# Optimization experiments

Hardware: AMD Instinct MI355X
Metric: run time of the kernel (lower is better)

## Reference

```python
import jax, jax.numpy as jnp
import numpy as np

D = 1024
H = 16
HD = D // H
FF = 4 * D

def layer_norm(x, g, b, eps=1e-5):
    mu = jnp.mean(x, axis=-1, keepdims=True)
    var = jnp.var(x, axis=-1, keepdims=True)
    return (x - mu) * jax.lax.rsqrt(var + eps) * g + b

def setup_inputs() -> dict:
    key = jax.random.key(0)
    ks = jax.random.split(key, 8)
    s = 0.02
    return {
        "x": jax.random.normal(ks[0], (2, 2048, D), jnp.float32),
        "ln1_g": jnp.ones((D,), jnp.float32),
        "ln1_b": jnp.zeros((D,), jnp.float32),
        "w_qkv": jax.random.normal(ks[1], (3 * D, D), jnp.float32) * s,
        "b_qkv": jnp.zeros((3 * D,), jnp.float32),
        "w_proj": jax.random.normal(ks[2], (D, D), jnp.float32) * s,
        "b_proj": jnp.zeros((D,), jnp.float32),
        "ln2_g": jnp.ones((D,), jnp.float32),
        "ln2_b": jnp.zeros((D,), jnp.float32),
        "w_fc1": jax.random.normal(ks[3], (FF, D), jnp.float32) * s,
        "b_fc1": jnp.zeros((FF,), jnp.float32),
        "w_fc2": jax.random.normal(ks[4], (D, FF), jnp.float32) * s,
        "b_fc2": jnp.zeros((D,), jnp.float32),
    }

def reference(x, ln1_g, ln1_b, w_qkv, b_qkv, w_proj, b_proj,
              ln2_g, ln2_b, w_fc1, b_fc1, w_fc2, b_fc2):
    B, N, C = x.shape
    scale = HD ** -0.5
    # --- attention branch (pre-norm) ---
    h = layer_norm(x, ln1_g, ln1_b)
    qkv = h @ w_qkv.T + b_qkv                      # [B,N,3D]
    qkv = qkv.reshape(B, N, 3, H, HD).transpose(2, 0, 3, 1, 4)
    q, k, v = qkv[0], qkv[1], qkv[2]               # [B,H,N,HD]
    attn = jnp.einsum('bhnd,bhmd->bhnm', q, k) * scale
    attn = jax.nn.softmax(attn, axis=-1)
    o = jnp.einsum('bhnm,bhmd->bhnd', attn, v)     # [B,H,N,HD]
    o = o.transpose(0, 2, 1, 3).reshape(B, N, C)
    x = x + (o @ w_proj.T + b_proj)
    # --- FFN branch (pre-norm) ---
    h = layer_norm(x, ln2_g, ln2_b)
    h = jax.nn.gelu(h @ w_fc1.T + b_fc1, approximate=False)
    x = x + (h @ w_fc2.T + b_fc2)
    return x
```

## Files before the change

kernel.cpp:

```cpp
#include <hip/hip_runtime.h>

typedef __attribute__((ext_vector_type(8))) short short8;
typedef __attribute__((ext_vector_type(4))) float f32x4;

static __device__ __forceinline__ unsigned short f2bf(float f){
  unsigned u = __float_as_uint(f);
  u += 0x7FFF + ((u >> 16) & 1);
  return (unsigned short)(u >> 16);
}

static __device__ __forceinline__ f32x4 MF(short8 a, short8 b, f32x4 c){
  return __builtin_amdgcn_mfma_f32_16x16x32_bf16(a, b, c, 0, 0, 0);
}

#define GL16(g, l) __builtin_amdgcn_global_load_lds( \
    (const __attribute__((address_space(1))) void*)(g), \
    (__attribute__((address_space(3))) void*)(l), 16, 0, 0)

#define SBAR { __builtin_amdgcn_sched_barrier(0); __builtin_amdgcn_s_barrier(); __builtin_amdgcn_sched_barrier(0); }

__global__ __launch_bounds__(256) void cvt_all(
    const float* __restrict__ a0, const float* __restrict__ a1,
    const float* __restrict__ a2, const float* __restrict__ a3,
    unsigned short* __restrict__ o0, unsigned short* __restrict__ o1,
    unsigned short* __restrict__ o2, unsigned short* __restrict__ o3){
  int i = blockIdx.x * 256 + threadIdx.x;
  const float* src; unsigned short* dst; int off;
  if (i < 786432)       { src = a0; dst = o0; off = i; }
  else if (i < 1048576) { src = a1; dst = o1; off = i - 786432; }
  else if (i < 2097152) { src = a2; dst = o2; off = i - 1048576; }
  else                  { src = a3; dst = o3; off = i - 2097152; }
  float4 v = reinterpret_cast<const float4*>(src)[off];
  ushort4 o;
  o.x = f2bf(v.x); o.y = f2bf(v.y); o.z = f2bf(v.z); o.w = f2bf(v.w);
  reinterpret_cast<ushort4*>(dst)[off] = o;
}

__global__ __launch_bounds__(256) void ln_bf16(const float* __restrict__ x,
    const float* __restrict__ g, const float* __restrict__ b,
    unsigned short* __restrict__ out){
  int row = blockIdx.x, t = threadIdx.x;
  const float* xr = x + (size_t)row * 1024;
  float4 xv = reinterpret_cast<const float4*>(xr)[t];
  float s  = xv.x + xv.y + xv.z + xv.w;
  float sq = xv.x*xv.x + xv.y*xv.y + xv.z*xv.z + xv.w*xv.w;
  #pragma unroll
  for (int m = 32; m >= 1; m >>= 1){ s += __shfl_xor(s, m); sq += __shfl_xor(sq, m); }
  __shared__ float ss[4], ssq[4];
  int w = t >> 6, lane = t & 63;
  if (lane == 0){ ss[w] = s; ssq[w] = sq; }
  __syncthreads();
  s  = ss[0] + ss[1] + ss[2] + ss[3];
  sq = ssq[0] + ssq[1] + ssq[2] + ssq[3];
  float mu = s * (1.f/1024.f);
  float rs = rsqrtf(sq * (1.f/1024.f) - mu*mu + 1e-5f);
  float4 gv = reinterpret_cast<const float4*>(g)[t];
  float4 bv = reinterpret_cast<const float4*>(b)[t];
  ushort4 o;
  o.x = f2bf((xv.x - mu) * rs * gv.x + bv.x);
  o.y = f2bf((xv.y - mu) * rs * gv.y + bv.y);
  o.z = f2bf((xv.z - mu) * rs * gv.z + bv.z);
  o.w = f2bf((xv.w - mu) * rs * gv.w + bv.w);
  reinterpret_cast<ushort4*>(out + (size_t)row * 1024)[t] = o;
}

template<int EPI>
__global__ __launch_bounds__(512, 2) void gemm8p(
    const unsigned short* __restrict__ A,
    const unsigned short* __restrict__ B,
    const float* __restrict__ bias,
    void* __restrict__ C,
    int M, int N, int K)
{
  __shared__ __attribute__((aligned(16))) short As[2 * 256 * 64];
  __shared__ __attribute__((aligned(16))) short Bs[2 * 256 * 64];
  const int NT = K >> 6;
  int tid = threadIdx.x, lane = tid & 63, wave = tid >> 6;
  int wm = wave >> 2, wn = wave & 3;
  int l15 = lane & 15, hi = lane >> 4;
  int hi2 = hi ^ (((l15 >> 2) & 1) << 1);
  int bm = blockIdx.y * 256, bn = blockIdx.x * 256;
  int lr = lane >> 3;
  int sg8 = ((lane & 7) ^ ((lane >> 5) << 1)) * 8;
  int rb0 = wave * 16;

  f32x4 acc[8][4] = {};
  short8 aR[4][2], bA[2][2], bB[2][2];

  auto stage = [&](int T, int h){
    if (T >= NT) return;
    const unsigned short* src = (h < 2) ? (A + (size_t)(bm + ((h & 1) << 7)) * K)
                                        : (B + (size_t)(bn + ((h & 1) << 7)) * K);
    short* dst = ((h < 2) ? As : Bs) + ((T & 1) << 14) + ((h & 1) << 13);
    const unsigned short* s = src + (size_t)(rb0 + lr) * K + (T << 6) + sg8;
    GL16(s, dst + rb0 * 64);
    GL16(s + (size_t)8 * K, dst + (rb0 + 8) * 64);
  };
  auto LDA = [&](const short* Ab, int m, int kk){
    int R = wm * 128 + m * 16 + l15;
    return *(const short8*)(Ab + R * 64 + kk * 32 + hi2 * 8);
  };
  auto LDB = [&](const short* Bb, int n, int kk){
    int R = wn * 64 + n * 16 + l15;
    return *(const short8*)(Bb + R * 64 + kk * 32 + hi2 * 8);
  };

  stage(0, 0); stage(0, 1); stage(0, 2); stage(0, 3);
  stage(1, 0); stage(1, 1);
  asm volatile("s_waitcnt vmcnt(4)" ::: "memory");
  SBAR;

  for (int i = 0; i < (NT >> 1); ++i){
    int t0 = 2 * i, t1 = t0 + 1;
    const short* A0 = As;            const short* B0 = Bs;
    const short* A1 = As + 16384;    const short* B1 = Bs + 16384;
    #pragma unroll
    for (int m = 0; m < 4; m++){ aR[m][0] = LDA(A0, m, 0); aR[m][1] = LDA(A0, m, 1); }
    #pragma unroll
    for (int n = 0; n < 2; n++){ bA[n][0] = LDB(B0, n, 0); bA[n][1] = LDB(B0, n, 1); }
    __builtin_amdgcn_sched_barrier(0);
    stage(t1, 2);
    SBAR;
    __builtin_amdgcn_s_setprio(1);
    #pragma unroll
    for (int m = 0; m < 4; m++)
      #pragma unroll
      for (int n = 0; n < 2; n++)
        #pragma unroll
        for (int kk = 0; kk < 2; kk++) acc[m][n] = MF(aR[m][kk], bA[n][kk], acc[m][n]);
    __builtin_amdgcn_s_setprio(0);
    SBAR;
    #pragma unroll
    for (int n = 0; n < 2; n++){ bB[n][0] = LDB(B0, n + 2, 0); bB[n][1] = LDB(B0, n + 2, 1); }
    __builtin_amdgcn_sched_barrier(0);
    stage(t1, 3);
    SBAR;
    __builtin_amdgcn_s_setprio(1);
    #pragma unroll
    for (int m = 0; m < 4; m++)
      #pragma unroll
      for (int n = 0; n < 2; n++)
        #pragma unroll
        for (int kk = 0; kk < 2; kk++) acc[m][n + 2] = MF(aR[m][kk], bB[n][kk], acc[m][n + 2]);
    __builtin_amdgcn_s_setprio(0);
    SBAR;
    #pragma unroll
    for (int m = 0; m < 4; m++){ aR[m][0] = LDA(A0, m + 4, 0); aR[m][1] = LDA(A0, m + 4, 1); }
    __builtin_amdgcn_sched_barrier(0);
    stage(t0 + 2, 0);
    SBAR;
    __builtin_amdgcn_s_setprio(1);
    #pragma unroll
    for (int m = 0; m < 4; m++)
      #pragma unroll
      for (int n = 0; n < 2; n++)
        #pragma unroll
        for (int kk = 0; kk < 2; kk++) acc[m + 4][n] = MF(aR[m][kk], bA[n][kk], acc[m + 4][n]);
    __builtin_amdgcn_s_setprio(0);
    SBAR;
    stage(t0 + 2, 1);
    SBAR;
    __builtin_amdgcn_s_setprio(1);
    #pragma unroll
    for (int m = 0; m < 4; m++)
      #pragma unroll
      for (int n = 0; n < 2; n++)
        #pragma unroll
        for (int kk = 0; kk < 2; kk++) acc[m + 4][n + 2] = MF(aR[m][kk], bB[n][kk], acc[m + 4][n + 2]);
    __builtin_amdgcn_s_setprio(0);
    asm volatile("s_waitcnt vmcnt(4)" ::: "memory");
    SBAR;
    #pragma unroll
    for (int m = 0; m < 4; m++){ aR[m][0] = LDA(A1, m, 0); aR[m][1] = LDA(A1, m, 1); }
    #pragma unroll
    for (int n = 0; n < 2; n++){ bA[n][0] = LDB(B1, n, 0); bA[n][1] = LDB(B1, n, 1); }
    __builtin_amdgcn_sched_barrier(0);
    stage(t0 + 2, 2);
    SBAR;
    __builtin_amdgcn_s_setprio(1);
    #pragma unroll
    for (int m = 0; m < 4; m++)
      #pragma unroll
      for (int n = 0; n < 2; n++)
        #pragma unroll
        for (int kk = 0; kk < 2; kk++) acc[m][n] = MF(aR[m][kk], bA[n][kk], acc[m][n]);
    __builtin_amdgcn_s_setprio(0);
    SBAR;
    #pragma unroll
    for (int n = 0; n < 2; n++){ bB[n][0] = LDB(B1, n + 2, 0); bB[n][1] = LDB(B1, n + 2, 1); }
    __builtin_amdgcn_sched_barrier(0);
    stage(t0 + 2, 3);
    SBAR;
    __builtin_amdgcn_s_setprio(1);
    #pragma unroll
    for (int m = 0; m < 4; m++)
      #pragma unroll
      for (int n = 0; n < 2; n++)
        #pragma unroll
        for (int kk = 0; kk < 2; kk++) acc[m][n + 2] = MF(aR[m][kk], bB[n][kk], acc[m][n + 2]);
    __builtin_amdgcn_s_setprio(0);
    SBAR;
    #pragma unroll
    for (int m = 0; m < 4; m++){ aR[m][0] = LDA(A1, m + 4, 0); aR[m][1] = LDA(A1, m + 4, 1); }
    __builtin_amdgcn_sched_barrier(0);
    stage(t0 + 3, 0);
    SBAR;
    __builtin_amdgcn_s_setprio(1);
    #pragma unroll
    for (int m = 0; m < 4; m++)
      #pragma unroll
      for (int n = 0; n < 2; n++)
        #pragma unroll
        for (int kk = 0; kk < 2; kk++) acc[m + 4][n] = MF(aR[m][kk], bA[n][kk], acc[m + 4][n]);
    __builtin_amdgcn_s_setprio(0);
    SBAR;
    stage(t0 + 3, 1);
    SBAR;
    __builtin_amdgcn_s_setprio(1);
    #pragma unroll
    for (int m = 0; m < 4; m++)
      #pragma unroll
      for (int n = 0; n < 2; n++)
        #pragma unroll
        for (int kk = 0; kk < 2; kk++) acc[m + 4][n + 2] = MF(aR[m][kk], bB[n][kk], acc[m + 4][n + 2]);
    __builtin_amdgcn_s_setprio(0);
    asm volatile("s_waitcnt vmcnt(4)" ::: "memory");
    SBAR;
  }

  #pragma unroll
  for (int m = 0; m < 8; m++){
    int row = bm + wm * 128 + m * 16 + hi * 4;
    #pragma unroll
    for (int n = 0; n < 4; n++){
      int col = bn + wn * 64 + n * 16 + l15;
      float bv = bias[col];
      #pragma unroll
      for (int j = 0; j < 4; j++){
        float v = acc[m][n][j] + bv;
        if (EPI == 1){
          float w2 = v * v;
          float t = exp2f(v * fmaf(w2, 0.10294322f, 2.3022078f));
          float r = __builtin_amdgcn_rcpf(1.f + t);
          v = v - v * r;
        }
        ((unsigned short*)C)[(size_t)(row + j) * N + col] = f2bf(v);
      }
    }
  }
}

template<int EPI>
__global__ __launch_bounds__(512) void gemm_ks(
    const unsigned short* __restrict__ A,
    const unsigned short* __restrict__ B,
    const float* __restrict__ bias,
    const float* __restrict__ resid,
    void* __restrict__ C,
    int M, int N, int K)
{
  __shared__ __attribute__((aligned(16))) short As[2][2][128 * 64];
  __shared__ __attribute__((aligned(16))) short Bs[2][2][128 * 64];
  const int NS = K >> 7;
  int tid = threadIdx.x, lane = tid & 63, wave = tid >> 6;
  int kg = wave >> 2;
  int ws = wave & 3;
  int wm = ws >> 1, wn = ws & 1;
  int l15 = lane & 15, hi = lane >> 4, l7 = l15 & 7;
  int lin = blockIdx.y * 8 + blockIdx.x;
  int xcd = lin & 7, idx = lin >> 3;
  int bm = (xcd * 4 + (idx >> 3)) * 128;
  int bn = (idx & 7) * 128;
  int lr = lane >> 3;
  int sega = ((lane & 7) ^ lr) * 8;
  f32x4 acc[4][4] = {};

  auto stage = [&](int buf, int k0){
    #pragma unroll
    for (int j = 0; j < 4; j++){
      int row = ws * 32 + j * 8;
      GL16(A + (size_t)(bm + row + lr) * K + k0 + sega, &As[kg][buf][row * 64]);
      GL16(B + (size_t)(bn + row + lr) * K + k0 + sega, &Bs[kg][buf][row * 64]);
    }
  };
  auto LDA = [&](int buf, int m, int kk){
    int R = wm * 64 + m * 16 + l15;
    return *(const short8*)(&As[kg][buf][R * 64 + (((kk << 2) | hi) ^ l7) * 8]);
  };
  auto LDB = [&](int buf, int n, int kk){
    int R = wn * 64 + n * 16 + l15;
    return *(const short8*)(&Bs[kg][buf][R * 64 + (((kk << 2) | hi) ^ l7) * 8]);
  };

  stage(0, kg * 64);
  for (int j = 0; j < NS; j++){
    int cur = j & 1;
    if (j + 1 < NS){
      stage(cur ^ 1, (j + 1) * 128 + kg * 64);
      asm volatile("s_waitcnt vmcnt(8)" ::: "memory");
    } else {
      asm volatile("s_waitcnt vmcnt(0)" ::: "memory");
    }
    SBAR;
    #pragma unroll
    for (int kk = 0; kk < 2; kk++){
      short8 af[4], bf[4];
      #pragma unroll
      for (int m = 0; m < 4; m++) af[m] = LDA(cur, m, kk);
      #pragma unroll
      for (int n = 0; n < 4; n++) bf[n] = LDB(cur, n, kk);
      __builtin_amdgcn_s_setprio(1);
      #pragma unroll
      for (int m = 0; m < 4; m++)
        #pragma unroll
        for (int n = 0; n < 4; n++)
          acc[m][n] = MF(af[m], bf[n], acc[m][n]);
      __builtin_amdgcn_s_setprio(0);
    }
    SBAR;
  }

  float* red = (float*)&As[0][0][0];
  if (kg == 1){
    #pragma unroll
    for (int m = 0; m < 4; m++)
      #pragma unroll
      for (int n = 0; n < 4; n++)
        #pragma unroll
        for (int j = 0; j < 4; j++)
          red[ws * 4096 + (m * 16 + hi * 4 + j) * 64 + n * 16 + l15] = acc[m][n][j];
  }
  __syncthreads();
  if (kg == 0){
    #pragma unroll
    for (int m = 0; m < 4; m++){
      int row = bm + wm * 64 + m * 16 + hi * 4;
      #pragma unroll
      for (int n = 0; n < 4; n++){
        int col = bn + wn * 64 + n * 16 + l15;
        float bv = bias[col];
        #pragma unroll
        for (int j = 0; j < 4; j++){
          float v = acc[m][n][j] + red[ws * 4096 + (m * 16 + hi * 4 + j) * 64 + n * 16 + l15] + bv;
          int r = row + j;
          if (EPI == 2){
            ((float*)C)[(size_t)r * N + col] = v + resid[(size_t)r * N + col];
          } else {
            ((unsigned short*)C)[(size_t)r * N + col] = f2bf(v);
          }
        }
      }
    }
  }
}

__global__ __launch_bounds__(512) void attn_fwd(const unsigned short* __restrict__ qkv,
                                                unsigned short* __restrict__ o){
  __shared__ __attribute__((aligned(16))) short K_lds[2][64*64];
  __shared__ __attribute__((aligned(16))) short V_lds[2][64*64];
  __shared__ __attribute__((aligned(16))) short P_lds[8][16*64];
  int tid = threadIdx.x, wave = tid >> 6, lane = tid & 63;
  int l15 = lane & 15, hi = lane >> 4, l7 = l15 & 7;
  int bid = blockIdx.x;
  int swz = (bid & 7) * 64 + (bid >> 3);
  int qt = swz & 15, bh = swz >> 4;
  int b = bh >> 4, h = bh & 15;
  const unsigned short* qbase = qkv + (size_t)b * 2048 * 3072 + h * 64;
  const unsigned short* kbase = qbase + 1024;
  const unsigned short* vbase = qbase + 2048;
  int qrow = qt * 128 + wave * 16 + l15;
  short8 qf0 = *(const short8*)(qbase + (size_t)qrow * 3072 + hi * 8);
  short8 qf1 = *(const short8*)(qbase + (size_t)qrow * 3072 + 32 + hi * 8);
  #pragma unroll
  for (int j = 0; j < 8; j++){
    float q0 = __uint_as_float((unsigned)(unsigned short)qf0[j] << 16) * 0.18033688f;
    float q1 = __uint_as_float((unsigned)(unsigned short)qf1[j] << 16) * 0.18033688f;
    qf0[j] = (short)f2bf(q0);
    qf1[j] = (short)f2bf(q1);
  }
  short8 ones8;
  #pragma unroll
  for (int j = 0; j < 8; j++) ones8[j] = (short)0x3F80;
  int vt = tid - 256;
  int ki0 = tid * 2, ki1 = ki0 + 1;
  int kr0 = ki0 >> 3, ks0 = ki0 & 7;
  int kr1 = ki1 >> 3, ks1 = ki1 & 7;
  int kp = vt & 31, ds8 = (vt >> 5) & 7;
  int vcg = kp >> 2, vwi = (2 * kp) & 7;
  f32x4 accO[4] = {};
  f32x4 lacc = {};
  short* Pw = &P_lds[wave][0];

  auto kv_load = [&](int kt, short8& s0, short8& s1){
    if (vt < 0){
      s0 = *(const short8*)(kbase + (size_t)(kt + kr0) * 3072 + ks0 * 8);
      s1 = *(const short8*)(kbase + (size_t)(kt + kr1) * 3072 + ks1 * 8);
    } else {
      const unsigned short* vr = vbase + (size_t)(kt + 2 * kp) * 3072 + ds8 * 8;
      s0 = *(const short8*)vr;
      s1 = *(const short8*)(vr + 3072);
    }
  };
  auto kv_store = [&](int buf, short8 s0, short8 s1){
    if (vt < 0){
      *(short8*)(&K_lds[buf][kr0 * 64 + ((ks0 ^ (kr0 & 7)) << 3)]) = s0;
      *(short8*)(&K_lds[buf][kr1 * 64 + ((ks1 ^ (kr1 & 7)) << 3)]) = s1;
    } else {
      unsigned* Vw = (unsigned*)&V_lds[buf][0];
      #pragma unroll
      for (int j = 0; j < 8; j++){
        int d = ds8 * 8 + j;
        int sa = d * 64 + ((vcg ^ (d & 7)) << 3) + vwi;
        Vw[sa >> 1] = (unsigned)(unsigned short)s0[j] | ((unsigned)(unsigned short)s1[j] << 16);
      }
    }
  };

  {
    short8 s0, s1;
    kv_load(0, s0, s1);
    kv_store(0, s0, s1);
    __syncthreads();
  }

  for (int t = 0; t < 32; t++){
    int cur = t & 1;
    const short* Kc = &K_lds[cur][0];
    const short* Vc = &V_lds[cur][0];
    short8 s0, s1;
    if (t < 31) kv_load((t + 1) * 64, s0, s1);
    f32x4 sacc[4];
    __builtin_amdgcn_s_setprio(1);
    #pragma unroll
    for (int kb = 0; kb < 4; kb++){
      f32x4 s = {};
      short8 ka = *(const short8*)(Kc + (kb * 16 + l15) * 64 + ((hi ^ l7) << 3));
      s = __builtin_amdgcn_mfma_f32_16x16x32_bf16(ka, qf0, s, 0, 0, 0);
      short8 kb_ = *(const short8*)(Kc + (kb * 16 + l15) * 64 + (((4 + hi) ^ l7) << 3));
      s = __builtin_amdgcn_mfma_f32_16x16x32_bf16(kb_, qf1, s, 0, 0, 0);
      sacc[kb] = s;
    }
    __builtin_amdgcn_s_setprio(0);
    unsigned pu[8];
    #pragma unroll
    for (int kb = 0; kb < 4; kb++){
      unsigned u0 = (unsigned)(int)fmaf(sacc[kb][0], 128.f, 16248.6f);
      unsigned u1 = (unsigned)(int)fmaf(sacc[kb][1], 128.f, 16248.6f);
      unsigned u2 = (unsigned)(int)fmaf(sacc[kb][2], 128.f, 16248.6f);
      unsigned u3 = (unsigned)(int)fmaf(sacc[kb][3], 128.f, 16248.6f);
      pu[kb * 2]     = u0 | (u1 << 16);
      pu[kb * 2 + 1] = u2 | (u3 << 16);
    }
    #pragma unroll
    for (int kb = 0; kb < 4; kb++){
      int sa = l15 * 64 + ((((kb << 1) | (hi >> 1)) ^ l7) << 3) + ((hi & 1) << 2);
      *(uint2*)(Pw + sa) = make_uint2(pu[kb * 2], pu[kb * 2 + 1]);
    }
    __builtin_amdgcn_s_setprio(1);
    #pragma unroll
    for (int kb2 = 0; kb2 < 2; kb2++){
      short8 pf = *(const short8*)(Pw + l15 * 64 + ((((kb2 << 2) | hi) ^ l7) << 3));
      #pragma unroll
      for (int db = 0; db < 4; db++){
        short8 vf = *(const short8*)(Vc + (db * 16 + l15) * 64 + ((((kb2 << 2) | hi) ^ l7) << 3));
        accO[db] = __builtin_amdgcn_mfma_f32_16x16x32_bf16(vf, pf, accO[db], 0, 0, 0);
      }
      lacc = __builtin_amdgcn_mfma_f32_16x16x32_bf16(ones8, pf, lacc, 0, 0, 0);
    }
    __builtin_amdgcn_s_setprio(0);
    if (t < 31){
      kv_store(cur ^ 1, s0, s1);
      __syncthreads();
    }
  }
  float inv = 1.f / lacc[0];
  unsigned short* ob = o + (size_t)(b * 2048 + qt * 128 + wave * 16 + l15) * 1024 + h * 64;
  #pragma unroll
  for (int db = 0; db < 4; db++){
    ushort4 w;
    w.x = f2bf(accO[db][0] * inv);
    w.y = f2bf(accO[db][1] * inv);
    w.z = f2bf(accO[db][2] * inv);
    w.w = f2bf(accO[db][3] * inv);
    *(ushort4*)(ob + db * 16 + hi * 4) = w;
  }
}

extern "C" void kernel_launch(void* const* d_in, const int* in_sizes, int n_in,
                              void* d_out, int out_size, void* d_ws, size_t ws_size,
                              hipStream_t stream){
  const float* x      = (const float*)d_in[0];
  const float* ln1_g  = (const float*)d_in[1];
  const float* ln1_b  = (const float*)d_in[2];
  const float* w_qkv  = (const float*)d_in[3];
  const float* b_qkv  = (const float*)d_in[4];
  const float* w_proj = (const float*)d_in[5];
  const float* b_proj = (const float*)d_in[6];
  const float* ln2_g  = (const float*)d_in[7];
  const float* ln2_b  = (const float*)d_in[8];
  const float* w_fc1  = (const float*)d_in[9];
  const float* b_fc1  = (const float*)d_in[10];
  const float* w_fc2  = (const float*)d_in[11];
  const float* b_fc2  = (const float*)d_in[12];
  float* out = (float*)d_out;
  char* ws = (char*)d_ws;
  const size_t MB = 1024 * 1024;
  unsigned short* h     = (unsigned short*)(ws);
  unsigned short* qkv   = (unsigned short*)(ws + 8*MB);
  unsigned short* ob    = (unsigned short*)(ws + 32*MB);
  float*          x1    = (float*)(ws + 40*MB);
  unsigned short* f     = (unsigned short*)(ws + 56*MB);
  unsigned short* wqkvb = (unsigned short*)(ws + 88*MB);
  unsigned short* wprojb= (unsigned short*)(ws + 94*MB);
  unsigned short* wfc1b = (unsigned short*)(ws + 96*MB);
  unsigned short* wfc2b = (unsigned short*)(ws + 104*MB);

  cvt_all<<<12288, 256, 0, stream>>>(w_qkv, w_proj, w_fc1, w_fc2,
                                     wqkvb, wprojb, wfc1b, wfc2b);

  ln_bf16<<<4096, 256, 0, stream>>>(x, ln1_g, ln1_b, h);
  gemm8p<0><<<dim3(12, 16), 512, 0, stream>>>(h, wqkvb, b_qkv, qkv, 4096, 3072, 1024);
  attn_fwd<<<512, 512, 0, stream>>>(qkv, ob);
  gemm_ks<2><<<dim3(8, 32), 512, 0, stream>>>(ob, wprojb, b_proj, x, x1, 4096, 1024, 1024);
  ln_bf16<<<4096, 256, 0, stream>>>(x1, ln2_g, ln2_b, h);
  gemm8p<1><<<dim3(16, 16), 512, 0, stream>>>(h, wfc1b, b_fc1, f, 4096, 4096, 1024);
  gemm_ks<2><<<dim3(8, 32), 512, 0, stream>>>(f, wfc2b, b_fc2, x1, out, 4096, 1024, 4096);
}
```

Measured before the change: 220.6 us.

## Run FC2 as split-K gemm8p with bf16 partials and separate reduce kernel

```diff
diff --git a/kernel.cpp b/kernel.cpp
--- a/kernel.cpp
+++ b/kernel.cpp
@@ -64,13 +64,32 @@
   reinterpret_cast<ushort4*>(out + (size_t)row * 1024)[t] = o;
 }
 
+__global__ __launch_bounds__(256) void reduce4(
+    const unsigned short* __restrict__ p, const float* __restrict__ bias,
+    const float* __restrict__ resid, float* __restrict__ out){
+  int i = blockIdx.x * 256 + threadIdx.x;
+  int e = i * 4, col = e & 1023;
+  float4 r = *reinterpret_cast<const float4*>(resid + e);
+  float4 bv = *reinterpret_cast<const float4*>(bias + col);
+  float s0 = r.x + bv.x, s1 = r.y + bv.y, s2 = r.z + bv.z, s3 = r.w + bv.w;
+  #pragma unroll
+  for (int sp = 0; sp < 4; sp++){
+    ushort4 u = *reinterpret_cast<const ushort4*>(p + (size_t)sp * 4194304 + e);
+    s0 += __uint_as_float((unsigned)u.x << 16);
+    s1 += __uint_as_float((unsigned)u.y << 16);
+    s2 += __uint_as_float((unsigned)u.z << 16);
+    s3 += __uint_as_float((unsigned)u.w << 16);
+  }
+  *reinterpret_cast<float4*>(out + e) = make_float4(s0, s1, s2, s3);
+}
+
 template<int EPI>
 __global__ __launch_bounds__(512, 2) void gemm8p(
     const unsigned short* __restrict__ A,
     const unsigned short* __restrict__ B,
     const float* __restrict__ bias,
     void* __restrict__ C,
-    int M, int N, int K)
+    int M, int N, int K, int LDK)
 {
   __shared__ __attribute__((aligned(16))) short As[2 * 256 * 64];
   __shared__ __attribute__((aligned(16))) short Bs[2 * 256 * 64];
@@ -80,6 +99,10 @@
   int l15 = lane & 15, hi = lane >> 4;
   int hi2 = hi ^ (((l15 >> 2) & 1) << 1);
   int bm = blockIdx.y * 256, bn = blockIdx.x * 256;
+  size_t koff = (size_t)blockIdx.z * K;
+  A += koff; B += koff;
+  unsigned short* Cp = (unsigned short*)C;
+  if (EPI == 3) Cp += (size_t)blockIdx.z * M * N;
   int lr = lane >> 3;
   int sg8 = ((lane & 7) ^ ((lane >> 5) << 1)) * 8;
   int rb0 = wave * 16;
@@ -89,12 +112,12 @@
 
   auto stage = [&](int T, int h){
     if (T >= NT) return;
-    const unsigned short* src = (h < 2) ? (A + (size_t)(bm + ((h & 1) << 7)) * K)
-                                        : (B + (size_t)(bn + ((h & 1) << 7)) * K);
+    const unsigned short* src = (h < 2) ? (A + (size_t)(bm + ((h & 1) << 7)) * LDK)
+                                        : (B + (size_t)(bn + ((h & 1) << 7)) * LDK);
     short* dst = ((h < 2) ? As : Bs) + ((T & 1) << 14) + ((h & 1) << 13);
-    const unsigned short* s = src + (size_t)(rb0 + lr) * K + (T << 6) + sg8;
+    const unsigned short* s = src + (size_t)(rb0 + lr) * LDK + (T << 6) + sg8;
     GL16(s, dst + rb0 * 64);
-    GL16(s + (size_t)8 * K, dst + (rb0 + 8) * 64);
+    GL16(s + (size_t)8 * LDK, dst + (rb0 + 8) * 64);
   };
   auto LDA = [&](const short* Ab, int m, int kk){
     int R = wm * 128 + m * 16 + l15;
@@ -234,7 +257,7 @@
     #pragma unroll
     for (int n = 0; n < 4; n++){
       int col = bn + wn * 64 + n * 16 + l15;
-      float bv = bias[col];
+      float bv = (EPI == 3) ? 0.f : bias[col];
       #pragma unroll
       for (int j = 0; j < 4; j++){
         float v = acc[m][n][j] + bv;
@@ -244,7 +267,7 @@
           float r = __builtin_amdgcn_rcpf(1.f + t);
           v = v - v * r;
         }
-        ((unsigned short*)C)[(size_t)(row + j) * N + col] = f2bf(v);
+        Cp[(size_t)(row + j) * N + col] = f2bf(v);
       }
     }
   }
@@ -514,15 +537,17 @@
   unsigned short* wprojb= (unsigned short*)(ws + 94*MB);
   unsigned short* wfc1b = (unsigned short*)(ws + 96*MB);
   unsigned short* wfc2b = (unsigned short*)(ws + 104*MB);
+  unsigned short* parts = (unsigned short*)(ws);
 
   cvt_all<<<12288, 256, 0, stream>>>(w_qkv, w_proj, w_fc1, w_fc2,
                                      wqkvb, wprojb, wfc1b, wfc2b);
 
   ln_bf16<<<4096, 256, 0, stream>>>(x, ln1_g, ln1_b, h);
-  gemm8p<0><<<dim3(12, 16), 512, 0, stream>>>(h, wqkvb, b_qkv, qkv, 4096, 3072, 1024);
+  gemm8p<0><<<dim3(12, 16), 512, 0, stream>>>(h, wqkvb, b_qkv, qkv, 4096, 3072, 1024, 1024);
   attn_fwd<<<512, 512, 0, stream>>>(qkv, ob);
   gemm_ks<2><<<dim3(8, 32), 512, 0, stream>>>(ob, wprojb, b_proj, x, x1, 4096, 1024, 1024);
   ln_bf16<<<4096, 256, 0, stream>>>(x1, ln2_g, ln2_b, h);
-  gemm8p<1><<<dim3(16, 16), 512, 0, stream>>>(h, wfc1b, b_fc1, f, 4096, 4096, 1024);
-  gemm_ks<2><<<dim3(8, 32), 512, 0, stream>>>(f, wfc2b, b_fc2, x1, out, 4096, 1024, 4096);
-}
+  gemm8p<1><<<dim3(16, 16), 512, 0, stream>>>(h, wfc1b, b_fc1, f, 4096, 4096, 1024, 1024);
+  gemm8p<3><<<dim3(4, 16, 4), 512, 0, stream>>>(f, wfc2b, nullptr, parts, 4096, 1024, 1024, 4096);
+  reduce4<<<4096, 256, 0, stream>>>(parts, b_fc2, x1, out);
+}
```

Result: no change. 224.8 us (+1.9%).
